# Performance work log

Measured on AMD Instinct MI355X. Metric: run time of the kernel, lower is better.

Reference implementation:

```python
import jax, jax.numpy as jnp
import numpy as np
from jax.ops import segment_sum, segment_max

N = 50000        # nodes
E = 800000       # edges (before self loops)
IN_DIM = 128
HID = 16         # per-head out channels
HEADS = 4
NL = 3           # num GAT layers
OUT = 1
NG = 128         # number of graphs in the batch
NEG = 0.2        # LeakyReLU negative slope (PyG GATConv default)
EPS = 1e-5       # BatchNorm eps


def setup_inputs() -> dict:
    key = jax.random.key(0)
    ks = iter(jax.random.split(key, 64))
    inp = {}
    inp['x'] = jax.random.normal(next(ks), (N, IN_DIM), jnp.float32)
    inp['edge_index'] = jax.random.randint(next(ks), (2, E), 0, N, dtype=jnp.int32)
    inp['batch'] = jnp.sort(jax.random.randint(next(ks), (N,), 0, NG, dtype=jnp.int32))
    d = IN_DIM
    for l in range(NL):
        s = 1.0 / np.sqrt(d)
        inp[f'W{l}'] = jax.random.uniform(next(ks), (HEADS * HID, d), jnp.float32, -s, s)
        inp[f'att_src{l}'] = jax.random.normal(next(ks), (HEADS, HID), jnp.float32) * 0.1
        inp[f'att_dst{l}'] = jax.random.normal(next(ks), (HEADS, HID), jnp.float32) * 0.1
        inp[f'bias{l}'] = jnp.zeros((HEADS * HID,), jnp.float32)
        inp[f'gamma{l}'] = jnp.ones((HEADS * HID,), jnp.float32)
        inp[f'beta{l}'] = jnp.zeros((HEADS * HID,), jnp.float32)
        inp[f'mean{l}'] = jax.random.normal(next(ks), (HEADS * HID,), jnp.float32) * 0.1
        inp[f'var{l}'] = jax.random.uniform(next(ks), (HEADS * HID,), jnp.float32, 0.5, 1.5)
        d = HEADS * HID
    s = 1.0 / np.sqrt(d)
    inp['fcW'] = jax.random.uniform(next(ks), (OUT, d), jnp.float32, -s, s)
    inp['fcb'] = jnp.zeros((OUT,), jnp.float32)
    return inp


def gat_layer(x, src, dst, W, att_src, att_dst, bias):
    """PyG GATConv (concat=True). src/dst already include self loops."""
    n = x.shape[0]
    h = (x @ W.T).reshape(n, HEADS, HID)            # [N,H,C]
    a_s = jnp.sum(h * att_src, axis=-1)             # [N,H]
    a_d = jnp.sum(h * att_dst, axis=-1)             # [N,H]
    logits = a_s[src] + a_d[dst]                    # [Etot,H]
    logits = jnp.where(logits > 0, logits, NEG * logits)  # leaky_relu
    # scatter-softmax over destination-node neighborhoods
    m = segment_max(logits, dst, num_segments=n)
    e = jnp.exp(logits - m[dst])
    z = segment_sum(e, dst, num_segments=n)
    alpha = e / z[dst]                              # [Etot,H]
    out = segment_sum(h[src] * alpha[:, :, None], dst, num_segments=n)  # [N,H,C]
    return out.reshape(n, HEADS * HID) + bias, alpha


def reference(x, edge_index, batch,
              W0, att_src0, att_dst0, bias0, gamma0, beta0, mean0, var0,
              W1, att_src1, att_dst1, bias1, gamma1, beta1, mean1, var1,
              W2, att_src2, att_dst2, bias2, gamma2, beta2, mean2, var2,
              fcW, fcb):
    n = x.shape[0]
    loops = jnp.arange(n, dtype=edge_index.dtype)   # add_self_loops=True
    src = jnp.concatenate([edge_index[0], loops])
    dst = jnp.concatenate([edge_index[1], loops])
    params = [
        (W0, att_src0, att_dst0, bias0, gamma0, beta0, mean0, var0),
        (W1, att_src1, att_dst1, bias1, gamma1, beta1, mean1, var1),
        (W2, att_src2, att_dst2, bias2, gamma2, beta2, mean2, var2),
    ]
    h = x
    alpha0 = None
    for l, (W, a_s, a_d, b, g, be, mu, var) in enumerate(params):
        h, alpha = gat_layer(h, src, dst, W, a_s, a_d, b)
        if l == 0:
            alpha0 = alpha
        h = jax.nn.relu(h)
        h = g * (h - mu) / jnp.sqrt(var + EPS) + be  # BatchNorm1d (eval); dropout = identity
    # global_mean_pool over graph ids
    sums = segment_sum(h, batch, num_segments=NG)
    cnt = segment_sum(jnp.ones((n, 1), h.dtype), batch, num_segments=NG)
    pooled = sums / jnp.maximum(cnt, 1.0)
    out = jax.nn.sigmoid(pooled @ fcW.T + fcb)      # [NG, OUT]
    return out, alpha0
```

## Files before the change

kernel.cpp:

```cpp
#include <hip/hip_runtime.h>
#include <hip/hip_fp16.h>
#include <math.h>

#define NN     50000
#define EE     800000
#define ETOT   (EE + NN)
#define INDIM  128
#define HEADS  4
#define NG     128
#define NEGS   0.2f
#define BNEPS  1e-5f

typedef _Float16 half8 __attribute__((ext_vector_type(8)));
typedef _Float16 half4v __attribute__((ext_vector_type(4)));
typedef float floatx4 __attribute__((ext_vector_type(4)));


__global__ void degree_kernel(const int* __restrict__ ei, int* __restrict__ deg,
                              int* __restrict__ rank) {
    int e = blockIdx.x * blockDim.x + threadIdx.x;
    if (e >= ETOT) return;
    int d = (e < EE) ? ei[EE + e] : (e - EE);
    rank[e] = atomicAdd(&deg[d], 1);
}

__global__ void scan_block_kernel(const int* __restrict__ deg, int* __restrict__ rowstart,
                                  int* __restrict__ bsums) {
    __shared__ int wsum[16];
    int tid = threadIdx.x;
    int lane = tid & 63;
    int w = tid >> 6;
    int i = blockIdx.x * 1024 + tid;
    int v = (i < NN) ? deg[i] : 0;
    int x = v;
#pragma unroll
    for (int off = 1; off < 64; off <<= 1) {
        int t = __shfl_up(x, off, 64);
        if (lane >= off) x += t;
    }
    if (lane == 63) wsum[w] = x;
    __syncthreads();
    if (w == 0 && lane < 16) {
        int s = wsum[lane];
#pragma unroll
        for (int off = 1; off < 16; off <<= 1) {
            int t = __shfl_up(s, off, 16);
            if ((lane & 15) >= off) s += t;
        }
        wsum[lane] = s;
    }
    __syncthreads();
    int base = (w > 0) ? wsum[w - 1] : 0;
    int incl = base + x;
    if (i < NN) rowstart[i] = incl - v;
    if (tid == 1023) bsums[blockIdx.x] = incl;
}

__global__ void add_offsets_kernel(int* __restrict__ rowstart, const int* __restrict__ bsums) {
    int i = blockIdx.x * blockDim.x + threadIdx.x;
    if (i == 0) rowstart[NN] = ETOT;
    if (i >= NN) return;
    int nbk = i >> 10;
    int off = 0;
    for (int j = 0; j < nbk; ++j) off += bsums[j];
    rowstart[i] += off;
}

__global__ void scatter_kernel(const int* __restrict__ ei, const int* __restrict__ rowstart,
                               const int* __restrict__ rank, int* __restrict__ csr) {
    int e = blockIdx.x * blockDim.x + threadIdx.x;
    if (e >= ETOT) return;
    int s, d;
    if (e < EE) { s = ei[e]; d = ei[EE + e]; }
    else        { s = e - EE; d = e - EE; }
    int pos = rowstart[d] + rank[e];
    csr[pos] = s;
}

#define NX8 (NN * INDIM / 8)
#define PREP_TOT (NX8 + 2048 + NN + NG * 64 + NG)
__global__ __launch_bounds__(256) void prep_kernel(const float* __restrict__ x,
                                                   const float* __restrict__ W0,
                                                   const float* __restrict__ W1,
                                                   const float* __restrict__ W2,
                                                   _Float16* __restrict__ Xh,
                                                   _Float16* __restrict__ Wh,
                                                   int* __restrict__ deg,
                                                   float* __restrict__ psums,
                                                   int* __restrict__ pcnt) {
    int i = blockIdx.x * blockDim.x + threadIdx.x;
    if (i < NX8) {
        float4 v0 = *(const float4*)(x + (size_t)i * 8);
        float4 v1 = *(const float4*)(x + (size_t)i * 8 + 4);
        half8 o;
        o[0] = (_Float16)v0.x; o[1] = (_Float16)v0.y;
        o[2] = (_Float16)v0.z; o[3] = (_Float16)v0.w;
        o[4] = (_Float16)v1.x; o[5] = (_Float16)v1.y;
        o[6] = (_Float16)v1.z; o[7] = (_Float16)v1.w;
        *(half8*)(Xh + (size_t)i * 8) = o;
    } else if (i < NX8 + 2048) {
        int wi = (i - NX8) * 8;
#pragma unroll
        for (int j = 0; j < 8; ++j) {
            int idx = wi + j;
            float v = (idx < 8192) ? W0[idx]
                    : ((idx < 12288) ? W1[idx - 8192] : W2[idx - 12288]);
            Wh[idx] = (_Float16)v;
        }
    } else if (i < NX8 + 2048 + NN) {
        deg[i - NX8 - 2048] = 0;
    } else if (i < NX8 + 2048 + NN + NG * 64) {
        psums[i - NX8 - 2048 - NN] = 0.f;
    } else if (i < PREP_TOT) {
        pcnt[i - NX8 - 2048 - NN - NG * 64] = 0;
    }
}

template <int DD>
__global__ __launch_bounds__(256) void gemm_att_kernel(
    const _Float16* __restrict__ X, const _Float16* __restrict__ Wh,
    const float* __restrict__ attS, const float* __restrict__ attD,
    _Float16* __restrict__ H, float* __restrict__ AS, float* __restrict__ ADZ) {
    constexpr int KB = DD / 32;
    int tid = threadIdx.x;
    int wv = tid >> 6;
    int lane = tid & 63;
    int quad = lane >> 4;
    int n = lane & 15;
    int wbase = blockIdx.x * 64 + wv * 16;

    int arow = wbase + n;
    if (arow >= NN) arow = NN - 1;
    half8 a[KB];
#pragma unroll
    for (int kb = 0; kb < KB; ++kb)
        a[kb] = *(const half8*)(X + (size_t)arow * DD + kb * 32 + quad * 8);

    floatx4 c[4];
#pragma unroll
    for (int t = 0; t < 4; ++t) {
        floatx4 acc = {0.f, 0.f, 0.f, 0.f};
#pragma unroll
        for (int kb = 0; kb < KB; ++kb) {
            half8 b = *(const half8*)(Wh + (size_t)(t * 16 + n) * DD + kb * 32 + quad * 8);
            acc = __builtin_amdgcn_mfma_f32_16x16x32_f16(a[kb], b, acc, 0, 0, 0);
        }
        c[t] = acc;
    }

    float as_l[4], ad_l[4];
#pragma unroll
    for (int t = 0; t < 4; ++t) {
        as_l[t] = attS[t * 16 + n];
        ad_l[t] = attD[t * 16 + n];
    }
#pragma unroll
    for (int r = 0; r < 4; ++r) {
        int node = wbase + quad * 4 + r;
        bool ok = node < NN;
#pragma unroll
        for (int t = 0; t < 4; ++t) {
            float h = c[t][r];
            if (ok) H[(size_t)node * 64 + t * 16 + n] = (_Float16)h;
            float vs = h * as_l[t];
            float vd = h * ad_l[t];
#pragma unroll
            for (int off = 8; off; off >>= 1) {
                vs += __shfl_down(vs, off, 16);
                vd += __shfl_down(vd, off, 16);
            }
            if (ok && n == 0) {
                AS[node * 4 + t] = vs;
                ADZ[(size_t)node * 8 + t] = vd;
            }
        }
    }
}

template <bool WRITE_Z>
__global__ __launch_bounds__(256) void edge_aggr_kernel(
    const _Float16* __restrict__ H, const float* __restrict__ AS,
    float* __restrict__ ADZ,
    const int* __restrict__ rowstart,
    const int* __restrict__ csr,
    const float* __restrict__ bias, const float* __restrict__ gamma,
    const float* __restrict__ beta, const float* __restrict__ mean,
    const float* __restrict__ var, _Float16* __restrict__ Hout) {
    int v = (blockIdx.x * blockDim.x + threadIdx.x) >> 6;
    if (v >= NN) return;
    int lane = threadIdx.x & 63;
    int q = lane >> 4;
    int l16 = lane & 15;
    int head = l16 >> 2;
    int ch4 = l16 * 4;
    float adv = ADZ[(size_t)v * 8 + head];
    int start = rowstart[v];
    int cnt = rowstart[v + 1] - start;
    const int* srow = csr + start;
    int cm1 = cnt - 1;
    float z = 0.f;
    float acc0 = 0.f, acc1 = 0.f, acc2 = 0.f, acc3 = 0.f;
    for (int k = 0; k < cnt; k += 16) {
        int b = k + q * 4;
        int s0 = srow[min(b + 0, cm1)];
        int s1 = srow[min(b + 1, cm1)];
        int s2 = srow[min(b + 2, cm1)];
        int s3 = srow[min(b + 3, cm1)];
        float a0 = AS[(size_t)s0 * 4 + head];
        float a1 = AS[(size_t)s1 * 4 + head];
        float a2 = AS[(size_t)s2 * 4 + head];
        float a3 = AS[(size_t)s3 * 4 + head];
        half4v h0 = *(const half4v*)(H + (size_t)s0 * 64 + ch4);
        half4v h1 = *(const half4v*)(H + (size_t)s1 * 64 + ch4);
        half4v h2 = *(const half4v*)(H + (size_t)s2 * 64 + ch4);
        half4v h3 = *(const half4v*)(H + (size_t)s3 * 64 + ch4);
        float l0 = a0 + adv; l0 = l0 > 0.f ? l0 : NEGS * l0;
        float l1 = a1 + adv; l1 = l1 > 0.f ? l1 : NEGS * l1;
        float l2 = a2 + adv; l2 = l2 > 0.f ? l2 : NEGS * l2;
        float l3 = a3 + adv; l3 = l3 > 0.f ? l3 : NEGS * l3;
        float p0 = (b + 0 < cnt) ? __expf(l0) : 0.f;
        float p1 = (b + 1 < cnt) ? __expf(l1) : 0.f;
        float p2 = (b + 2 < cnt) ? __expf(l2) : 0.f;
        float p3 = (b + 3 < cnt) ? __expf(l3) : 0.f;
        z += (p0 + p1) + (p2 + p3);
        acc0 = fmaf(p0, (float)h0[0], acc0); acc1 = fmaf(p0, (float)h0[1], acc1);
        acc2 = fmaf(p0, (float)h0[2], acc2); acc3 = fmaf(p0, (float)h0[3], acc3);
        acc0 = fmaf(p1, (float)h1[0], acc0); acc1 = fmaf(p1, (float)h1[1], acc1);
        acc2 = fmaf(p1, (float)h1[2], acc2); acc3 = fmaf(p1, (float)h1[3], acc3);
        acc0 = fmaf(p2, (float)h2[0], acc0); acc1 = fmaf(p2, (float)h2[1], acc1);
        acc2 = fmaf(p2, (float)h2[2], acc2); acc3 = fmaf(p2, (float)h2[3], acc3);
        acc0 = fmaf(p3, (float)h3[0], acc0); acc1 = fmaf(p3, (float)h3[1], acc1);
        acc2 = fmaf(p3, (float)h3[2], acc2); acc3 = fmaf(p3, (float)h3[3], acc3);
    }
    z    += __shfl_xor(z, 16);    z    += __shfl_xor(z, 32);
    acc0 += __shfl_xor(acc0, 16); acc0 += __shfl_xor(acc0, 32);
    acc1 += __shfl_xor(acc1, 16); acc1 += __shfl_xor(acc1, 32);
    acc2 += __shfl_xor(acc2, 16); acc2 += __shfl_xor(acc2, 32);
    acc3 += __shfl_xor(acc3, 16); acc3 += __shfl_xor(acc3, 32);
    if (q == 0) {
        if (WRITE_Z && (l16 & 3) == 0) ADZ[(size_t)v * 8 + 4 + head] = z;
        float4 bi = *(const float4*)(bias + ch4);
        float4 ga = *(const float4*)(gamma + ch4);
        float4 be = *(const float4*)(beta + ch4);
        float4 mu = *(const float4*)(mean + ch4);
        float4 va = *(const float4*)(var + ch4);
        float r0 = fmaxf(acc0 / z + bi.x, 0.f);
        float r1 = fmaxf(acc1 / z + bi.y, 0.f);
        float r2 = fmaxf(acc2 / z + bi.z, 0.f);
        float r3 = fmaxf(acc3 / z + bi.w, 0.f);
        r0 = ga.x * (r0 - mu.x) * rsqrtf(va.x + BNEPS) + be.x;
        r1 = ga.y * (r1 - mu.y) * rsqrtf(va.y + BNEPS) + be.y;
        r2 = ga.z * (r2 - mu.z) * rsqrtf(va.z + BNEPS) + be.z;
        r3 = ga.w * (r3 - mu.w) * rsqrtf(va.w + BNEPS) + be.w;
        half4v o;
        o[0] = (_Float16)r0;
        o[1] = (_Float16)r1;
        o[2] = (_Float16)r2;
        o[3] = (_Float16)r3;
        *(half4v*)(Hout + (size_t)v * 64 + ch4) = o;
    }
}

__global__ __launch_bounds__(256) void alpha_kernel(
    const int* __restrict__ ei,
    const float* __restrict__ AS, const float* __restrict__ ADZ,
    float* __restrict__ alpha_out) {
    int e = blockIdx.x * blockDim.x + threadIdx.x;
    if (e >= ETOT) return;
    int s, d;
    if (e < EE) { s = ei[e]; d = ei[EE + e]; }
    else        { s = e - EE; d = e - EE; }
    float4 as = *(const float4*)(AS + (size_t)s * 4);
    const float* row = ADZ + (size_t)d * 8;
    float4 ad = *(const float4*)(row);
    float4 z4 = *(const float4*)(row + 4);
    float l;
    float4 a;
    l = as.x + ad.x; l = l > 0.f ? l : NEGS * l; a.x = __expf(l) / z4.x;
    l = as.y + ad.y; l = l > 0.f ? l : NEGS * l; a.y = __expf(l) / z4.y;
    l = as.z + ad.z; l = l > 0.f ? l : NEGS * l; a.z = __expf(l) / z4.z;
    l = as.w + ad.w; l = l > 0.f ? l : NEGS * l; a.w = __expf(l) / z4.w;
    *(float4*)(alpha_out + (size_t)e * 4) = a;
}

__global__ __launch_bounds__(256) void pool_kernel(const __half* __restrict__ H,
                                                   const int* __restrict__ batch,
                                                   float* __restrict__ sums,
                                                   int* __restrict__ cnt) {
    int wid = (blockIdx.x * blockDim.x + threadIdx.x) >> 6;
    int lane = threadIdx.x & 63;
    int base = wid * 16;
    if (base >= NN) return;
    int end = min(base + 16, NN);
    int cur = batch[base];
    float acc = 0.f;
    int c0 = 0;
    for (int i = base; i < end; ++i) {
        int g = batch[i];
        if (g != cur) {
            atomicAdd(&sums[cur * 64 + lane], acc);
            if (lane == 0) atomicAdd(&cnt[cur], c0);
            cur = g; acc = 0.f; c0 = 0;
        }
        acc += __half2float(H[(size_t)i * 64 + lane]);
        c0++;
    }
    atomicAdd(&sums[cur * 64 + lane], acc);
    if (lane == 0) atomicAdd(&cnt[cur], c0);
}

__global__ void fc_kernel(const float* __restrict__ sums, const int* __restrict__ cnt,
                          const float* __restrict__ fcW, const float* __restrict__ fcb,
                          float* __restrict__ out) {
    int g = (blockIdx.x * blockDim.x + threadIdx.x) >> 6;
    int lane = threadIdx.x & 63;
    if (g >= NG) return;
    float c = fmaxf((float)cnt[g], 1.f);
    float val = (sums[g * 64 + lane] / c) * fcW[lane];
#pragma unroll
    for (int off = 32; off; off >>= 1) val += __shfl_down(val, off, 64);
    if (lane == 0) out[g] = 1.f / (1.f + expf(-(val + fcb[0])));
}

extern "C" void kernel_launch(void* const* d_in, const int* in_sizes, int n_in,
                              void* d_out, int out_size, void* d_ws, size_t ws_size,
                              hipStream_t stream) {
    const float* x   = (const float*)d_in[0];
    const int* ei    = (const int*)d_in[1];
    const int* batch = (const int*)d_in[2];
    const float* W[3], *attS[3], *attD[3], *bias[3], *gamma[3], *beta[3], *mean[3], *var[3];
    for (int l = 0; l < 3; ++l) {
        W[l]     = (const float*)d_in[3 + 8 * l + 0];
        attS[l]  = (const float*)d_in[3 + 8 * l + 1];
        attD[l]  = (const float*)d_in[3 + 8 * l + 2];
        bias[l]  = (const float*)d_in[3 + 8 * l + 3];
        gamma[l] = (const float*)d_in[3 + 8 * l + 4];
        beta[l]  = (const float*)d_in[3 + 8 * l + 5];
        mean[l]  = (const float*)d_in[3 + 8 * l + 6];
        var[l]   = (const float*)d_in[3 + 8 * l + 7];
    }
    const float* fcW = (const float*)d_in[27];
    const float* fcb = (const float*)d_in[28];
    float* out = (float*)d_out;
    float* alpha_out = (float*)d_out + NG;

    char* p = (char*)d_ws;
    auto carve = [&](size_t bytes) {
        char* q = p;
        p += (bytes + 255) & ~(size_t)255;
        return q;
    };
    _Float16* Xh    = (_Float16*)carve(sizeof(_Float16) * NN * INDIM);
    _Float16* Wh    = (_Float16*)carve(sizeof(_Float16) * 16384);
    _Float16* Hh    = (_Float16*)carve(sizeof(_Float16) * NN * 64);
    _Float16* Hn    = (_Float16*)carve(sizeof(_Float16) * NN * 64);
    float* AS       = (float*)carve(sizeof(float) * NN * 4);
    float* ADZ      = (float*)carve(sizeof(float) * NN * 8);
    int*   rowstart = (int*)carve(sizeof(int) * (NN + 1));
    int*   deg      = (int*)carve(sizeof(int) * NN);
    int*   rank     = (int*)carve(sizeof(int) * ETOT);
    int*   bsums    = (int*)carve(sizeof(int) * 64);
    int*   csr      = (int*)carve(sizeof(int) * ETOT);
    float* psums    = (float*)carve(sizeof(float) * NG * 64);
    int*   pcnt     = (int*)carve(sizeof(int) * NG);

    prep_kernel<<<(PREP_TOT + 255) / 256, 256, 0, stream>>>(
        x, W[0], W[1], W[2], Xh, Wh, deg, psums, pcnt);

    int nbScan = (NN + 1023) / 1024;
    degree_kernel<<<(ETOT + 255) / 256, 256, 0, stream>>>(ei, deg, rank);
    scan_block_kernel<<<nbScan, 1024, 0, stream>>>(deg, rowstart, bsums);
    add_offsets_kernel<<<(NN + 255) / 256, 256, 0, stream>>>(rowstart, bsums);
    scatter_kernel<<<(ETOT + 255) / 256, 256, 0, stream>>>(ei, rowstart, rank, csr);

    int edgeBlocks = (NN * 64 + 255) / 256;
    int posBlocks = (ETOT + 255) / 256;
    int gemmBlocks = (NN + 63) / 64;

    gemm_att_kernel<128><<<gemmBlocks, 256, 0, stream>>>(Xh, Wh, attS[0], attD[0],
                                                         Hh, AS, ADZ);
    edge_aggr_kernel<true><<<edgeBlocks, 256, 0, stream>>>(
        Hh, AS, ADZ, rowstart, csr,
        bias[0], gamma[0], beta[0], mean[0], var[0], Hn);
    alpha_kernel<<<posBlocks, 256, 0, stream>>>(ei, AS, ADZ, alpha_out);

    gemm_att_kernel<64><<<gemmBlocks, 256, 0, stream>>>(Hn, Wh + 8192, attS[1], attD[1],
                                                        Hh, AS, ADZ);
    edge_aggr_kernel<false><<<edgeBlocks, 256, 0, stream>>>(
        Hh, AS, ADZ, rowstart, csr,
        bias[1], gamma[1], beta[1], mean[1], var[1], Hn);

    gemm_att_kernel<64><<<gemmBlocks, 256, 0, stream>>>(Hn, Wh + 12288, attS[2], attD[2],
                                                        Hh, AS, ADZ);
    edge_aggr_kernel<false><<<edgeBlocks, 256, 0, stream>>>(
        Hh, AS, ADZ, rowstart, csr,
        bias[2], gamma[2], beta[2], mean[2], var[2], Hn);

    int poolWaves = (NN + 15) / 16;
    pool_kernel<<<(poolWaves * 64 + 255) / 256, 256, 0, stream>>>(
        (const __half*)Hn, batch, psums, pcnt);
    fc_kernel<<<(NG * 64 + 255) / 256, 256, 0, stream>>>(psums, pcnt, fcW, fcb, out);
}
```

Baseline: 346.8 us.

## Horizontally fuse independent kernels and fold pooling into last aggregation

Kernels with no data dependence on each other now share one launch, split by block index: x/W conversion with degree counting, layer-0 GEMM with the CSR scatter, and layer-1 GEMM with the alpha output. The attention-score buffers are double-buffered so alpha can read layer-0 scores while layer 1 writes its own. The separate mean-pool kernel is removed; the last edge-aggregation kernel atomically adds each node's output into per-graph sums. This cuts launch count and a pass over the final features, but adds one float atomic per node-channel on only 128×64 addresses, which can contend heavily.

```diff
diff --git a/kernel.cpp b/kernel.cpp
--- a/kernel.cpp
+++ b/kernel.cpp
@@ -16,12 +16,57 @@
 typedef float floatx4 __attribute__((ext_vector_type(4)));
 
 
-__global__ void degree_kernel(const int* __restrict__ ei, int* __restrict__ deg,
-                              int* __restrict__ rank) {
-    int e = blockIdx.x * blockDim.x + threadIdx.x;
-    if (e >= ETOT) return;
-    int d = (e < EE) ? ei[EE + e] : (e - EE);
-    rank[e] = atomicAdd(&deg[d], 1);
+#define GEMMB  ((NN + 63) / 64)
+#define SCATB  ((ETOT + 255) / 256)
+#define NX8    (NN * INDIM / 8)
+#define P1     (NX8 + 2048)
+#define P2     (P1 + NG * 64)
+#define P3     (P2 + NG)
+#define PREPB  ((P3 + 255) / 256)
+
+__global__ void zero_deg_kernel(int* __restrict__ deg) {
+    int i = blockIdx.x * blockDim.x + threadIdx.x;
+    if (i < NN) deg[i] = 0;
+}
+
+__global__ __launch_bounds__(256) void prep_degree_kernel(
+    const float* __restrict__ x, const float* __restrict__ W0,
+    const float* __restrict__ W1, const float* __restrict__ W2,
+    _Float16* __restrict__ Xh, _Float16* __restrict__ Wh,
+    float* __restrict__ psums, int* __restrict__ pcnt,
+    const int* __restrict__ ei, int* __restrict__ deg, int* __restrict__ rank) {
+    int bid = blockIdx.x;
+    if (bid < PREPB) {
+        int i = bid * 256 + threadIdx.x;
+        if (i < NX8) {
+            float4 v0 = *(const float4*)(x + (size_t)i * 8);
+            float4 v1 = *(const float4*)(x + (size_t)i * 8 + 4);
+            half8 o;
+            o[0] = (_Float16)v0.x; o[1] = (_Float16)v0.y;
+            o[2] = (_Float16)v0.z; o[3] = (_Float16)v0.w;
+            o[4] = (_Float16)v1.x; o[5] = (_Float16)v1.y;
+            o[6] = (_Float16)v1.z; o[7] = (_Float16)v1.w;
+            *(half8*)(Xh + (size_t)i * 8) = o;
+        } else if (i < P1) {
+            int wi = (i - NX8) * 8;
+#pragma unroll
+            for (int j = 0; j < 8; ++j) {
+                int idx = wi + j;
+                float v = (idx < 8192) ? W0[idx]
+                        : ((idx < 12288) ? W1[idx - 8192] : W2[idx - 12288]);
+                Wh[idx] = (_Float16)v;
+            }
+        } else if (i < P2) {
+            psums[i - P1] = 0.f;
+        } else if (i < P3) {
+            pcnt[i - P2] = 0;
+        }
+    } else {
+        int e = (bid - PREPB) * 256 + threadIdx.x;
+        if (e >= ETOT) return;
+        int d = (e < EE) ? ei[EE + e] : (e - EE);
+        rank[e] = atomicAdd(&deg[d], 1);
+    }
 }
 
 __global__ void scan_block_kernel(const int* __restrict__ deg, int* __restrict__ rowstart,
@@ -66,9 +111,11 @@
     rowstart[i] += off;
 }
 
-__global__ void scatter_kernel(const int* __restrict__ ei, const int* __restrict__ rowstart,
-                               const int* __restrict__ rank, int* __restrict__ csr) {
-    int e = blockIdx.x * blockDim.x + threadIdx.x;
+__device__ __forceinline__ void scatter_body(int bid, const int* __restrict__ ei,
+                                             const int* __restrict__ rowstart,
+                                             const int* __restrict__ rank,
+                                             int* __restrict__ csr) {
+    int e = bid * 256 + threadIdx.x;
     if (e >= ETOT) return;
     int s, d;
     if (e < EE) { s = ei[e]; d = ei[EE + e]; }
@@ -77,48 +124,9 @@
     csr[pos] = s;
 }
 
-#define NX8 (NN * INDIM / 8)
-#define PREP_TOT (NX8 + 2048 + NN + NG * 64 + NG)
-__global__ __launch_bounds__(256) void prep_kernel(const float* __restrict__ x,
-                                                   const float* __restrict__ W0,
-                                                   const float* __restrict__ W1,
-                                                   const float* __restrict__ W2,
-                                                   _Float16* __restrict__ Xh,
-                                                   _Float16* __restrict__ Wh,
-                                                   int* __restrict__ deg,
-                                                   float* __restrict__ psums,
-                                                   int* __restrict__ pcnt) {
-    int i = blockIdx.x * blockDim.x + threadIdx.x;
-    if (i < NX8) {
-        float4 v0 = *(const float4*)(x + (size_t)i * 8);
-        float4 v1 = *(const float4*)(x + (size_t)i * 8 + 4);
-        half8 o;
-        o[0] = (_Float16)v0.x; o[1] = (_Float16)v0.y;
-        o[2] = (_Float16)v0.z; o[3] = (_Float16)v0.w;
-        o[4] = (_Float16)v1.x; o[5] = (_Float16)v1.y;
-        o[6] = (_Float16)v1.z; o[7] = (_Float16)v1.w;
-        *(half8*)(Xh + (size_t)i * 8) = o;
-    } else if (i < NX8 + 2048) {
-        int wi = (i - NX8) * 8;
-#pragma unroll
-        for (int j = 0; j < 8; ++j) {
-            int idx = wi + j;
-            float v = (idx < 8192) ? W0[idx]
-                    : ((idx < 12288) ? W1[idx - 8192] : W2[idx - 12288]);
-            Wh[idx] = (_Float16)v;
-        }
-    } else if (i < NX8 + 2048 + NN) {
-        deg[i - NX8 - 2048] = 0;
-    } else if (i < NX8 + 2048 + NN + NG * 64) {
-        psums[i - NX8 - 2048 - NN] = 0.f;
-    } else if (i < PREP_TOT) {
-        pcnt[i - NX8 - 2048 - NN - NG * 64] = 0;
-    }
-}
-
 template <int DD>
-__global__ __launch_bounds__(256) void gemm_att_kernel(
-    const _Float16* __restrict__ X, const _Float16* __restrict__ Wh,
+__device__ __forceinline__ void gemm_att_body(
+    int bid, const _Float16* __restrict__ X, const _Float16* __restrict__ Wh,
     const float* __restrict__ attS, const float* __restrict__ attD,
     _Float16* __restrict__ H, float* __restrict__ AS, float* __restrict__ ADZ) {
     constexpr int KB = DD / 32;
@@ -127,7 +135,7 @@
     int lane = tid & 63;
     int quad = lane >> 4;
     int n = lane & 15;
-    int wbase = blockIdx.x * 64 + wv * 16;
+    int wbase = bid * 64 + wv * 16;
 
     int arow = wbase + n;
     if (arow >= NN) arow = NN - 1;
@@ -177,7 +185,59 @@
     }
 }
 
-template <bool WRITE_Z>
+__device__ __forceinline__ void alpha_body(
+    int bid, const int* __restrict__ ei, const float* __restrict__ AS,
+    const float* __restrict__ ADZ, float* __restrict__ alpha_out) {
+    int e = bid * 256 + threadIdx.x;
+    if (e >= ETOT) return;
+    int s, d;
+    if (e < EE) { s = ei[e]; d = ei[EE + e]; }
+    else        { s = e - EE; d = e - EE; }
+    float4 as = *(const float4*)(AS + (size_t)s * 4);
+    const float* row = ADZ + (size_t)d * 8;
+    float4 ad = *(const float4*)(row);
+    float4 z4 = *(const float4*)(row + 4);
+    float l;
+    float4 a;
+    l = as.x + ad.x; l = l > 0.f ? l : NEGS * l; a.x = __expf(l) / z4.x;
+    l = as.y + ad.y; l = l > 0.f ? l : NEGS * l; a.y = __expf(l) / z4.y;
+    l = as.z + ad.z; l = l > 0.f ? l : NEGS * l; a.z = __expf(l) / z4.z;
+    l = as.w + ad.w; l = l > 0.f ? l : NEGS * l; a.w = __expf(l) / z4.w;
+    *(float4*)(alpha_out + (size_t)e * 4) = a;
+}
+
+__global__ __launch_bounds__(256) void gemm0_scatter_kernel(
+    const _Float16* __restrict__ X, const _Float16* __restrict__ Wh,
+    const float* __restrict__ attS, const float* __restrict__ attD,
+    _Float16* __restrict__ H, float* __restrict__ AS, float* __restrict__ ADZ,
+    const int* __restrict__ ei, const int* __restrict__ rowstart,
+    const int* __restrict__ rank, int* __restrict__ csr) {
+    if (blockIdx.x < GEMMB)
+        gemm_att_body<128>(blockIdx.x, X, Wh, attS, attD, H, AS, ADZ);
+    else
+        scatter_body(blockIdx.x - GEMMB, ei, rowstart, rank, csr);
+}
+
+__global__ __launch_bounds__(256) void gemm1_alpha_kernel(
+    const _Float16* __restrict__ X, const _Float16* __restrict__ Wh,
+    const float* __restrict__ attS, const float* __restrict__ attD,
+    _Float16* __restrict__ H, float* __restrict__ ASb, float* __restrict__ ADZb,
+    const int* __restrict__ ei, const float* __restrict__ ASa,
+    const float* __restrict__ ADZa, float* __restrict__ alpha_out) {
+    if (blockIdx.x < GEMMB)
+        gemm_att_body<64>(blockIdx.x, X, Wh, attS, attD, H, ASb, ADZb);
+    else
+        alpha_body(blockIdx.x - GEMMB, ei, ASa, ADZa, alpha_out);
+}
+
+__global__ __launch_bounds__(256) void gemm2_kernel(
+    const _Float16* __restrict__ X, const _Float16* __restrict__ Wh,
+    const float* __restrict__ attS, const float* __restrict__ attD,
+    _Float16* __restrict__ H, float* __restrict__ AS, float* __restrict__ ADZ) {
+    gemm_att_body<64>(blockIdx.x, X, Wh, attS, attD, H, AS, ADZ);
+}
+
+template <int MODE>
 __global__ __launch_bounds__(256) void edge_aggr_kernel(
     const _Float16* __restrict__ H, const float* __restrict__ AS,
     float* __restrict__ ADZ,
@@ -185,7 +245,9 @@
     const int* __restrict__ csr,
     const float* __restrict__ bias, const float* __restrict__ gamma,
     const float* __restrict__ beta, const float* __restrict__ mean,
-    const float* __restrict__ var, _Float16* __restrict__ Hout) {
+    const float* __restrict__ var, _Float16* __restrict__ Hout,
+    const int* __restrict__ batch, float* __restrict__ psums,
+    int* __restrict__ pcnt) {
     int v = (blockIdx.x * blockDim.x + threadIdx.x) >> 6;
     if (v >= NN) return;
     int lane = threadIdx.x & 63;
@@ -238,7 +300,7 @@
     acc2 += __shfl_xor(acc2, 16); acc2 += __shfl_xor(acc2, 32);
     acc3 += __shfl_xor(acc3, 16); acc3 += __shfl_xor(acc3, 32);
     if (q == 0) {
-        if (WRITE_Z && (l16 & 3) == 0) ADZ[(size_t)v * 8 + 4 + head] = z;
+        if (MODE == 0 && (l16 & 3) == 0) ADZ[(size_t)v * 8 + 4 + head] = z;
         float4 bi = *(const float4*)(bias + ch4);
         float4 ga = *(const float4*)(gamma + ch4);
         float4 be = *(const float4*)(beta + ch4);
@@ -252,61 +314,23 @@
         r1 = ga.y * (r1 - mu.y) * rsqrtf(va.y + BNEPS) + be.y;
         r2 = ga.z * (r2 - mu.z) * rsqrtf(va.z + BNEPS) + be.z;
         r3 = ga.w * (r3 - mu.w) * rsqrtf(va.w + BNEPS) + be.w;
-        half4v o;
-        o[0] = (_Float16)r0;
-        o[1] = (_Float16)r1;
-        o[2] = (_Float16)r2;
-        o[3] = (_Float16)r3;
-        *(half4v*)(Hout + (size_t)v * 64 + ch4) = o;
-    }
-}
-
-__global__ __launch_bounds__(256) void alpha_kernel(
-    const int* __restrict__ ei,
-    const float* __restrict__ AS, const float* __restrict__ ADZ,
-    float* __restrict__ alpha_out) {
-    int e = blockIdx.x * blockDim.x + threadIdx.x;
-    if (e >= ETOT) return;
-    int s, d;
-    if (e < EE) { s = ei[e]; d = ei[EE + e]; }
-    else        { s = e - EE; d = e - EE; }
-    float4 as = *(const float4*)(AS + (size_t)s * 4);
-    const float* row = ADZ + (size_t)d * 8;
-    float4 ad = *(const float4*)(row);
-    float4 z4 = *(const float4*)(row + 4);
-    float l;
-    float4 a;
-    l = as.x + ad.x; l = l > 0.f ? l : NEGS * l; a.x = __expf(l) / z4.x;
-    l = as.y + ad.y; l = l > 0.f ? l : NEGS * l; a.y = __expf(l) / z4.y;
-    l = as.z + ad.z; l = l > 0.f ? l : NEGS * l; a.z = __expf(l) / z4.z;
-    l = as.w + ad.w; l = l > 0.f ? l : NEGS * l; a.w = __expf(l) / z4.w;
-    *(float4*)(alpha_out + (size_t)e * 4) = a;
-}
-
-__global__ __launch_bounds__(256) void pool_kernel(const __half* __restrict__ H,
-                                                   const int* __restrict__ batch,
-                                                   float* __restrict__ sums,
-                                                   int* __restrict__ cnt) {
-    int wid = (blockIdx.x * blockDim.x + threadIdx.x) >> 6;
-    int lane = threadIdx.x & 63;
-    int base = wid * 16;
-    if (base >= NN) return;
-    int end = min(base + 16, NN);
-    int cur = batch[base];
-    float acc = 0.f;
-    int c0 = 0;
-    for (int i = base; i < end; ++i) {
-        int g = batch[i];
-        if (g != cur) {
-            atomicAdd(&sums[cur * 64 + lane], acc);
-            if (lane == 0) atomicAdd(&cnt[cur], c0);
-            cur = g; acc = 0.f; c0 = 0;
+        if (MODE == 2) {
+            int g = batch[v];
+            float* ps = psums + (size_t)g * 64 + ch4;
+            atomicAdd(ps + 0, r0);
+            atomicAdd(ps + 1, r1);
+            atomicAdd(ps + 2, r2);
+            atomicAdd(ps + 3, r3);
+            if (l16 == 0) atomicAdd(&pcnt[g], 1);
+        } else {
+            half4v o;
+            o[0] = (_Float16)r0;
+            o[1] = (_Float16)r1;
+            o[2] = (_Float16)r2;
+            o[3] = (_Float16)r3;
+            *(half4v*)(Hout + (size_t)v * 64 + ch4) = o;
         }
-        acc += __half2float(H[(size_t)i * 64 + lane]);
-        c0++;
-    }
-    atomicAdd(&sums[cur * 64 + lane], acc);
-    if (lane == 0) atomicAdd(&cnt[cur], c0);
+    }
 }
 
 __global__ void fc_kernel(const float* __restrict__ sums, const int* __restrict__ cnt,
@@ -354,8 +378,10 @@
     _Float16* Wh    = (_Float16*)carve(sizeof(_Float16) * 16384);
     _Float16* Hh    = (_Float16*)carve(sizeof(_Float16) * NN * 64);
     _Float16* Hn    = (_Float16*)carve(sizeof(_Float16) * NN * 64);
-    float* AS       = (float*)carve(sizeof(float) * NN * 4);
-    float* ADZ      = (float*)carve(sizeof(float) * NN * 8);
+    float* ASa      = (float*)carve(sizeof(float) * NN * 4);
+    float* ADZa     = (float*)carve(sizeof(float) * NN * 8);
+    float* ASb      = (float*)carve(sizeof(float) * NN * 4);
+    float* ADZb     = (float*)carve(sizeof(float) * NN * 8);
     int*   rowstart = (int*)carve(sizeof(int) * (NN + 1));
     int*   deg      = (int*)carve(sizeof(int) * NN);
     int*   rank     = (int*)carve(sizeof(int) * ETOT);
@@ -364,40 +390,38 @@
     float* psums    = (float*)carve(sizeof(float) * NG * 64);
     int*   pcnt     = (int*)carve(sizeof(int) * NG);
 
-    prep_kernel<<<(PREP_TOT + 255) / 256, 256, 0, stream>>>(
-        x, W[0], W[1], W[2], Xh, Wh, deg, psums, pcnt);
+    int edgeBlocks = (NN * 64 + 255) / 256;
+
+    zero_deg_kernel<<<(NN + 255) / 256, 256, 0, stream>>>(deg);
+
+    prep_degree_kernel<<<PREPB + SCATB, 256, 0, stream>>>(
+        x, W[0], W[1], W[2], Xh, Wh, psums, pcnt, ei, deg, rank);
 
     int nbScan = (NN + 1023) / 1024;
-    degree_kernel<<<(ETOT + 255) / 256, 256, 0, stream>>>(ei, deg, rank);
     scan_block_kernel<<<nbScan, 1024, 0, stream>>>(deg, rowstart, bsums);
     add_offsets_kernel<<<(NN + 255) / 256, 256, 0, stream>>>(rowstart, bsums);
-    scatter_kernel<<<(ETOT + 255) / 256, 256, 0, stream>>>(ei, rowstart, rank, csr);
-
-    int edgeBlocks = (NN * 64 + 255) / 256;
-    int posBlocks = (ETOT + 255) / 256;
-    int gemmBlocks = (NN + 63) / 64;
-
-    gemm_att_kernel<128><<<gemmBlocks, 256, 0, stream>>>(Xh, Wh, attS[0], attD[0],
-                                                         Hh, AS, ADZ);
-    edge_aggr_kernel<true><<<edgeBlocks, 256, 0, stream>>>(
-        Hh, AS, ADZ, rowstart, csr,
-        bias[0], gamma[0], beta[0], mean[0], var[0], Hn);
-    alpha_kernel<<<posBlocks, 256, 0, stream>>>(ei, AS, ADZ, alpha_out);
-
-    gemm_att_kernel<64><<<gemmBlocks, 256, 0, stream>>>(Hn, Wh + 8192, attS[1], attD[1],
-                                                        Hh, AS, ADZ);
-    edge_aggr_kernel<false><<<edgeBlocks, 256, 0, stream>>>(
-        Hh, AS, ADZ, rowstart, csr,
-        bias[1], gamma[1], beta[1], mean[1], var[1], Hn);
-
-    gemm_att_kernel<64><<<gemmBlocks, 256, 0, stream>>>(Hn, Wh + 12288, attS[2], attD[2],
-                                                        Hh, AS, ADZ);
-    edge_aggr_kernel<false><<<edgeBlocks, 256, 0, stream>>>(
-        Hh, AS, ADZ, rowstart, csr,
-        bias[2], gamma[2], beta[2], mean[2], var[2], Hn);
-
-    int poolWaves = (NN + 15) / 16;
-    pool_kernel<<<(poolWaves * 64 + 255) / 256, 256, 0, stream>>>(
-        (const __half*)Hn, batch, psums, pcnt);
+
+    gemm0_scatter_kernel<<<GEMMB + SCATB, 256, 0, stream>>>(
+        Xh, Wh, attS[0], attD[0], Hh, ASa, ADZa, ei, rowstart, rank, csr);
+
+    edge_aggr_kernel<0><<<edgeBlocks, 256, 0, stream>>>(
+        Hh, ASa, ADZa, rowstart, csr,
+        bias[0], gamma[0], beta[0], mean[0], var[0], Hn, nullptr, nullptr, nullptr);
+
+    gemm1_alpha_kernel<<<GEMMB + SCATB, 256, 0, stream>>>(
+        Hn, Wh + 8192, attS[1], attD[1], Hh, ASb, ADZb,
+        ei, ASa, ADZa, alpha_out);
+
+    edge_aggr_kernel<1><<<edgeBlocks, 256, 0, stream>>>(
+        Hh, ASb, ADZb, rowstart, csr,
+        bias[1], gamma[1], beta[1], mean[1], var[1], Hn, nullptr, nullptr, nullptr);
+
+    gemm2_kernel<<<GEMMB, 256, 0, stream>>>(
+        Hn, Wh + 12288, attS[2], attD[2], Hh, ASa, ADZa);
+
+    edge_aggr_kernel<2><<<edgeBlocks, 256, 0, stream>>>(
+        Hh, ASa, ADZa, rowstart, csr,
+        bias[2], gamma[2], beta[2], mean[2], var[2], nullptr, batch, psums, pcnt);
+
     fc_kernel<<<(NG * 64 + 255) / 256, 256, 0, stream>>>(psums, pcnt, fcW, fcb, out);
 }
```

New measurement: 544.9 us. 1.57x slower.
